# Kernel optimization log

Hardware: AMD Instinct MI355X
Metric: run time of the kernel (lower is better)

Reference implementation:

```python
import jax, jax.numpy as jnp
import numpy as np

EPS = 1e-5


def conv1x1(x, w, b=None):
    # x: [B,C,H,W], w: [O,C] (1x1 conv kernel squeezed)
    y = jnp.einsum('bchw,oc->bohw', x, w)
    if b is not None:
        y = y + b[None, :, None, None]
    return y


def bn_inf(x, g, b, m, v):
    scale = g / jnp.sqrt(v + EPS)
    return (x - m[None, :, None, None]) * scale[None, :, None, None] + b[None, :, None, None]


def setup_inputs() -> dict:
    B, C, H, W = 2, 256, 80, 80
    Ck, Cv, Co = 64, 128, 256
    key = jax.random.key(0)
    ks = jax.random.split(key, 16)
    d = {}
    d['x'] = jax.random.normal(ks[0], (B, C, H, W), dtype=jnp.float32)
    d['y'] = jax.random.normal(ks[1], (B, C, H, W), dtype=jnp.float32)
    s = 1.0 / np.sqrt(C)
    d['fk_w'] = jax.random.normal(ks[2], (Ck, C), dtype=jnp.float32) * s
    d['fk_g'] = jnp.ones((Ck,), jnp.float32)
    d['fk_b'] = jnp.zeros((Ck,), jnp.float32)
    d['fk_m'] = jax.random.normal(ks[3], (Ck,), dtype=jnp.float32) * 0.1
    d['fk_v'] = jax.random.uniform(ks[4], (Ck,), minval=0.5, maxval=1.5, dtype=jnp.float32)
    d['fq_w'] = jax.random.normal(ks[5], (Ck, C), dtype=jnp.float32) * s
    d['fq_g'] = jnp.ones((Ck,), jnp.float32)
    d['fq_b'] = jnp.zeros((Ck,), jnp.float32)
    d['fq_m'] = jax.random.normal(ks[6], (Ck,), dtype=jnp.float32) * 0.1
    d['fq_v'] = jax.random.uniform(ks[7], (Ck,), minval=0.5, maxval=1.5, dtype=jnp.float32)
    d['fv_w'] = jax.random.normal(ks[8], (Cv, C), dtype=jnp.float32) * s
    d['fv_b'] = jnp.zeros((Cv,), jnp.float32)
    d['W_w'] = jax.random.normal(ks[9], (Co, Cv), dtype=jnp.float32) * (1.0 / np.sqrt(Cv))
    d['W_b'] = jnp.zeros((Co,), jnp.float32)
    d['gamma'] = jnp.array([0.5], jnp.float32)
    return d


def reference(x, y, fk_w, fk_g, fk_b, fk_m, fk_v, fq_w, fq_g, fq_b, fq_m, fq_v, fv_w, fv_b, W_w, W_b, gamma):
    B, C, H, W = x.shape
    Ck = fk_w.shape[0]
    Cv = fv_w.shape[0]
    N = H * W
    # key from x, query/value from y (1x1 conv + BN projections)
    k = bn_inf(conv1x1(x, fk_w), fk_g, fk_b, fk_m, fk_v).reshape(B, Ck, N)          # [B,Ck,N]
    q = bn_inf(conv1x1(y, fq_w), fq_g, fq_b, fq_m, fq_v).reshape(B, Ck, N)          # [B,Ck,N]
    v = conv1x1(y, fv_w, fv_b).reshape(B, Cv, N)                                     # [B,Cv,N]
    sim = jnp.einsum('bkn,bkm->bnm', q, k) * (Ck ** -0.5)                            # [B,N,N]
    sim = jax.nn.softmax(sim, axis=-1)
    ctx = jnp.einsum('bnm,bvm->bvn', sim, v).reshape(B, Cv, H, W)                    # [B,Cv,H,W]
    ctx = conv1x1(ctx, W_w, W_b)                                                     # [B,Co,H,W]
    return gamma[0] * ctx + x
```

## Files before the change

kernel.cpp:

```cpp
#include <hip/hip_runtime.h>
#include <math.h>

#define NB   2
#define CIN  256
#define NN   6400
#define CKd  64
#define CVd  128
#define COd  256

using bf16   = __bf16;
using bf16x4 = __attribute__((ext_vector_type(4))) bf16;
using bf16x8 = __attribute__((ext_vector_type(8))) bf16;
using f32x4  = __attribute__((ext_vector_type(4))) float;

__device__ __forceinline__ void lds_cp16(const void* g, void* l) {
    __builtin_amdgcn_global_load_lds((const __attribute__((address_space(1))) void*)g,
                                     (__attribute__((address_space(3))) void*)l, 16, 0, 0);
}

__global__ void prep_kernel(const float* __restrict__ fk_w, const float* __restrict__ fk_g,
                            const float* __restrict__ fk_b, const float* __restrict__ fk_m,
                            const float* __restrict__ fk_v,
                            const float* __restrict__ fq_w, const float* __restrict__ fq_g,
                            const float* __restrict__ fq_b, const float* __restrict__ fq_m,
                            const float* __restrict__ fq_v,
                            const float* __restrict__ fv_w, const float* __restrict__ fv_b,
                            const float* __restrict__ W_w,  const float* __restrict__ W_b,
                            bf16* __restrict__ wkb, bf16* __restrict__ wqb,
                            bf16* __restrict__ wvb, bf16* __restrict__ wob,
                            float* __restrict__ bias)
{
    const int idx = blockIdx.x * 256 + threadIdx.x;
    const float QS = 0.18033688011112042f;
    if (idx < 16384) {
        const int co = idx >> 8;
        const float a = fk_g[co] * rsqrtf(fk_v[co] + 1e-5f);
        wkb[idx] = (bf16)(fk_w[idx] * a);
    } else if (idx < 32768) {
        const int i = idx - 16384, co = i >> 8;
        const float a = fq_g[co] * rsqrtf(fq_v[co] + 1e-5f) * QS;
        wqb[i] = (bf16)(fq_w[i] * a);
    } else if (idx < 65536) {
        const int i = idx - 32768;
        wvb[i] = (bf16)fv_w[i];
    } else if (idx < 98304) {
        const int i = idx - 65536;
        wob[i] = (bf16)W_w[i];
    } else if (idx < 98816) {
        const int j = idx - 98304;
        if (j < 64)       { const float a = fk_g[j] * rsqrtf(fk_v[j] + 1e-5f); bias[j] = fk_b[j] - fk_m[j] * a; }
        else if (j < 128) { const int c = j - 64; const float a = fq_g[c] * rsqrtf(fq_v[c] + 1e-5f); bias[j] = (fq_b[c] - fq_m[c] * a) * QS; }
        else if (j < 256) bias[j] = fv_b[j - 128];
        else              bias[j] = W_b[j - 256];
    }
}

__launch_bounds__(256, 4)
__global__ void projkqv_kernel(const float* __restrict__ x, const float* __restrict__ y,
                               const bf16* __restrict__ wkb, const bf16* __restrict__ wqb,
                               const bf16* __restrict__ wvb, const float* __restrict__ bias,
                               bf16* __restrict__ kb, bf16* __restrict__ qb, bf16* __restrict__ vb)
{
    __shared__ __align__(16) bf16 sbuf[64 * 128];
    __shared__ __align__(16) bf16 wbuf[64 * 128];

    const int tid  = threadIdx.x;
    const int lane = tid & 63, wav = tid >> 6;
    const int l15  = lane & 15, quad = lane >> 4;
    const int b    = blockIdx.z, m = blockIdx.y;
    const int n0   = blockIdx.x * 64;

    const float* srcg = ((m == 0) ? x : y) + (size_t)b * CIN * NN;
    const bf16* wg    = (m == 0) ? wkb : (m == 1) ? wqb : (wvb + (size_t)(m - 2) * 64 * CIN);

    const int key = l15 & 7;
    f32x4 acc[4];
#pragma unroll
    for (int j = 0; j < 4; ++j) acc[j] = (f32x4){0.f, 0.f, 0.f, 0.f};

    for (int p = 0; p < 2; ++p) {
        if (p) __syncthreads();

        {
            const int r4  = lane >> 4;
            const int c16 = lane & 15;
#pragma unroll
            for (int i = 0; i < 4; ++i) {
                const int rg = wav * 16 + i * 4;
                const int r  = rg + r4;
                const int cs = c16 ^ (r & 7);
                lds_cp16(wg + (size_t)r * 256 + p * 128 + cs * 8, &wbuf[rg * 128]);
            }
        }
        {
            const int nl = (tid & 15) * 4;
            const int cq = tid >> 4;
            const int cb = p * 128 + cq * 8;
            float4 v[8];
#pragma unroll
            for (int e = 0; e < 8; ++e)
                v[e] = *(const float4*)(srcg + (size_t)(cb + e) * NN + n0 + nl);
#pragma unroll
            for (int i = 0; i < 4; ++i) {
                const int n = nl + i;
                bf16x8 pk;
#pragma unroll
                for (int e = 0; e < 8; ++e) pk[e] = (bf16)(&v[e].x)[i];
                *(bf16x8*)&sbuf[n * 128 + ((cq ^ (n & 7)) * 8)] = pk;
            }
        }
        __syncthreads();

        if (m < 2) {
            const int arow = wav * 16 + l15;
#pragma unroll
            for (int k4 = 0; k4 < 16; k4 += 4) {
                const bf16x8 af = *(const bf16x8*)&sbuf[arow * 128 + (((k4 + quad) ^ key) * 8)];
#pragma unroll
                for (int nt = 0; nt < 4; ++nt) {
                    const int brow = nt * 16 + l15;
                    const bf16x8 bfw = *(const bf16x8*)&wbuf[brow * 128 + (((k4 + quad) ^ key) * 8)];
                    acc[nt] = __builtin_amdgcn_mfma_f32_16x16x32_bf16(af, bfw, acc[nt], 0, 0, 0);
                }
            }
        } else {
            const int arow = wav * 16 + l15;
#pragma unroll
            for (int k4 = 0; k4 < 16; k4 += 4) {
                const bf16x8 af = *(const bf16x8*)&wbuf[arow * 128 + (((k4 + quad) ^ key) * 8)];
#pragma unroll
                for (int nt = 0; nt < 4; ++nt) {
                    const int brow = nt * 16 + l15;
                    const bf16x8 bfy = *(const bf16x8*)&sbuf[brow * 128 + (((k4 + quad) ^ key) * 8)];
                    acc[nt] = __builtin_amdgcn_mfma_f32_16x16x32_bf16(af, bfy, acc[nt], 0, 0, 0);
                }
            }
        }
    }

    if (m < 2) {
        const float* bs = bias + m * 64;
        bf16* dst = (m == 0) ? kb : qb;
        const int nb = n0 + wav * 16;
#pragma unroll
        for (int nt = 0; nt < 4; ++nt) {
            const float bv = bs[nt * 16 + l15];
#pragma unroll
            for (int r = 0; r < 4; ++r) {
                const int n = nb + quad * 4 + r;
                dst[((size_t)b * NN + n) * CKd + nt * 16 + l15] = (bf16)(acc[nt][r] + bv);
            }
        }
    } else {
        const int cv0 = (m - 2) * 64 + wav * 16;
#pragma unroll
        for (int r = 0; r < 4; ++r) {
            const int cv = cv0 + quad * 4 + r;
            const float bv = bias[128 + cv];
#pragma unroll
            for (int nt = 0; nt < 4; ++nt)
                vb[((size_t)b * CVd + cv) * NN + n0 + nt * 16 + l15] = (bf16)(acc[nt][r] + bv);
        }
    }
}

__launch_bounds__(256, 2)
__global__ void attn_kernel(const bf16* __restrict__ qb, const bf16* __restrict__ kb,
                            const bf16* __restrict__ vb,
                            bf16* __restrict__ pO, float* __restrict__ pl, int KS)
{
    __shared__ __align__(16) bf16 kbuf[2][64 * 64];
    __shared__ __align__(16) bf16 vbuf[2][128 * 64];
    __shared__ __align__(16) bf16 p_lds[4][2][2][16][64];

    const int lane = threadIdx.x & 63;
    const int wav  = threadIdx.x >> 6;
    const int l15  = lane & 15;
    const int quad = lane >> 4;
    const int r8   = lane >> 3;
    const int c_src = (lane & 7) ^ r8;
    const int sw   = l15 & 7;
    const int pkey = (l15 & 7) << 1;

    const int id    = blockIdx.x;
    const int ks    = id % KS;
    const int rst   = id / KS;
    const int b     = rst & 1;
    const int qtile = rst >> 1;
    const int q0    = qtile * 256 + wav * 64;

    const bf16* qrow = qb + (size_t)b * NN * CKd;
    const bf16* krow = kb + (size_t)b * NN * CKd;
    const bf16* vrow = vb + (size_t)b * CVd * NN;

    bf16x8 qf[4][2];
#pragma unroll
    for (int qt = 0; qt < 4; ++qt)
#pragma unroll
        for (int s = 0; s < 2; ++s)
            qf[qt][s] = *(const bf16x8*)(qrow + (size_t)(q0 + qt * 16 + l15) * CKd + s * 32 + quad * 8);

    const float ZC = -11.541560327111707f;
    const f32x4 zini = (f32x4){ZC, ZC, ZC, ZC};

    f32x4 acc[4][8];
#pragma unroll
    for (int qt = 0; qt < 4; ++qt)
#pragma unroll
        for (int cv = 0; cv < 8; ++cv) acc[qt][cv] = (f32x4){0.f, 0.f, 0.f, 0.f};
    float psum[4] = {0.f, 0.f, 0.f, 0.f};

    const int t0 = (100 * ks) / KS;
    const int nt = (100 * (ks + 1)) / KS - t0;

    auto stage = [&](int t, int bi) {
        const int key0 = t * 64;
        lds_cp16(krow + (size_t)(key0 + wav * 8 + r8) * CKd + c_src * 8,
                 &kbuf[bi][(wav * 8) * 64]);
        lds_cp16(krow + (size_t)(key0 + (wav + 4) * 8 + r8) * CKd + c_src * 8,
                 &kbuf[bi][((wav + 4) * 8) * 64]);
#pragma unroll
        for (int g4 = 0; g4 < 4; ++g4) {
            const int g = wav * 4 + g4;
            lds_cp16(vrow + (size_t)(g * 8 + r8) * NN + key0 + c_src * 8,
                     &vbuf[bi][(g * 8) * 64]);
        }
    };

    stage(t0, 0);

    for (int t = 0; t < nt; ++t) {
        __syncthreads();
        if (t + 1 < nt) stage(t0 + t + 1, (t + 1) & 1);
        const bf16* kcur = &kbuf[t & 1][0];
        const bf16* vcur = &vbuf[t & 1][0];

        f32x4 s4[2][4];

        __builtin_amdgcn_s_setprio(1);
#pragma unroll
        for (int kt = 0; kt < 4; ++kt) {
            const int rr = kt * 16 + l15;
            const bf16x8 kf0 = *(const bf16x8*)&kcur[rr * 64 + ((quad ^ sw) * 8)];
            const bf16x8 kf1 = *(const bf16x8*)&kcur[rr * 64 + (((4 + quad) ^ sw) * 8)];
#pragma unroll
            for (int qtl = 0; qtl < 2; ++qtl) {
                f32x4 z = zini;
                z = __builtin_amdgcn_mfma_f32_16x16x32_bf16(kf0, qf[qtl][0], z, 0, 0, 0);
                z = __builtin_amdgcn_mfma_f32_16x16x32_bf16(kf1, qf[qtl][1], z, 0, 0, 0);
                s4[qtl][kt] = z;
            }
        }
        __builtin_amdgcn_s_setprio(0);

#pragma unroll
        for (int qtl = 0; qtl < 2; ++qtl) {
            float ps = 0.f;
#pragma unroll
            for (int kt = 0; kt < 4; ++kt) {
                bf16x4 pk;
#pragma unroll
                for (int r = 0; r < 4; ++r) {
                    const float p = exp2f(s4[qtl][kt][r]);
                    ps += p;
                    pk[r] = (bf16)p;
                }
                *(bf16x4*)&p_lds[wav][0][qtl][l15][((kt * 4 + quad) ^ pkey) * 4] = pk;
            }
            psum[qtl] += ps;
        }

        __builtin_amdgcn_s_setprio(1);
#pragma unroll
        for (int kt = 0; kt < 4; ++kt) {
            const int rr = kt * 16 + l15;
            const bf16x8 kf0 = *(const bf16x8*)&kcur[rr * 64 + ((quad ^ sw) * 8)];
            const bf16x8 kf1 = *(const bf16x8*)&kcur[rr * 64 + (((4 + quad) ^ sw) * 8)];
#pragma unroll
            for (int qtl = 0; qtl < 2; ++qtl) {
                f32x4 z = zini;
                z = __builtin_amdgcn_mfma_f32_16x16x32_bf16(kf0, qf[2 + qtl][0], z, 0, 0, 0);
                z = __builtin_amdgcn_mfma_f32_16x16x32_bf16(kf1, qf[2 + qtl][1], z, 0, 0, 0);
                s4[qtl][kt] = z;
            }
        }
        __builtin_amdgcn_s_setprio(0);

        {
            bf16x8 pfA, pfB;
#pragma unroll
            for (int u = 0; u < 8; ++u) {
                const int sp = u >> 2;
                if ((u & 3) == 0) {
                    pfA = *(const bf16x8*)&p_lds[wav][0][0][l15][((sp * 8 + quad * 2) ^ pkey) * 4];
                    pfB = *(const bf16x8*)&p_lds[wav][0][1][l15][((sp * 8 + quad * 2) ^ pkey) * 4];
                }
                {
                    const int qtl = u >> 2, kt = u & 3;
                    bf16x4 pk;
                    float ps = 0.f;
#pragma unroll
                    for (int r = 0; r < 4; ++r) {
                        const float p = exp2f(s4[qtl][kt][r]);
                        ps += p;
                        pk[r] = (bf16)p;
                    }
                    *(bf16x4*)&p_lds[wav][1][qtl][l15][((kt * 4 + quad) ^ pkey) * 4] = pk;
                    psum[2 + qtl] += ps;
                }
#pragma unroll
                for (int v2 = 0; v2 < 2; ++v2) {
                    const int cvt = (u & 3) * 2 + v2;
                    const int rr = cvt * 16 + l15;
                    const bf16x8 vf = *(const bf16x8*)&vcur[rr * 64 + (((sp * 4 + quad) ^ sw) * 8)];
                    acc[0][cvt] = __builtin_amdgcn_mfma_f32_16x16x32_bf16(vf, pfA, acc[0][cvt], 0, 0, 0);
                    acc[1][cvt] = __builtin_amdgcn_mfma_f32_16x16x32_bf16(vf, pfB, acc[1][cvt], 0, 0, 0);
                }
            }
        }

        __builtin_amdgcn_s_setprio(1);
#pragma unroll
        for (int sp = 0; sp < 2; ++sp) {
            const bf16x8 pf0 = *(const bf16x8*)&p_lds[wav][1][0][l15][((sp * 8 + quad * 2) ^ pkey) * 4];
            const bf16x8 pf1 = *(const bf16x8*)&p_lds[wav][1][1][l15][((sp * 8 + quad * 2) ^ pkey) * 4];
#pragma unroll
            for (int cvt = 0; cvt < 8; ++cvt) {
                const int rr = cvt * 16 + l15;
                const bf16x8 vf = *(const bf16x8*)&vcur[rr * 64 + (((sp * 4 + quad) ^ sw) * 8)];
                acc[2][cvt] = __builtin_amdgcn_mfma_f32_16x16x32_bf16(vf, pf0, acc[2][cvt], 0, 0, 0);
                acc[3][cvt] = __builtin_amdgcn_mfma_f32_16x16x32_bf16(vf, pf1, acc[3][cvt], 0, 0, 0);
            }
        }
        __builtin_amdgcn_s_setprio(0);
    }

    __syncthreads();
    bf16* tbuf = &p_lds[wav][0][0][0][0];
    const size_t pb = (size_t)ks * NB + b;
#pragma unroll
    for (int qt = 0; qt < 4; ++qt) {
        psum[qt] += __shfl_xor(psum[qt], 16);
        psum[qt] += __shfl_xor(psum[qt], 32);
#pragma unroll
        for (int cvt = 0; cvt < 8; ++cvt) {
            bf16x4 pk;
#pragma unroll
            for (int r = 0; r < 4; ++r) pk[r] = (bf16)acc[qt][cvt][r];
            const int u = (cvt * 4 + quad) ^ (l15 << 1);
            *(bf16x4*)&tbuf[l15 * 128 + u * 4] = pk;
        }
#pragma unroll
        for (int j = 0; j < 4; ++j) {
            const int row = j * 4 + (lane >> 4);
            const int g   = ((lane & 15) * 2) ^ ((row & 15) << 1);
            const bf16x8 vv = *(const bf16x8*)&tbuf[row * 128 + g * 4];
            *(bf16x8*)(pO + (pb * NN + q0 + qt * 16) * CVd + j * 512 + lane * 8) = vv;
        }
        if (quad == 0) pl[pb * NN + q0 + qt * 16 + l15] = psum[qt];
    }
}

__launch_bounds__(256, 4)
__global__ void outproj_kernel(const bf16* __restrict__ pO, const float* __restrict__ pl,
                               const bf16* __restrict__ wob, const float* __restrict__ bias,
                               const float* __restrict__ x, const float* __restrict__ gam,
                               float* __restrict__ out, int KS)
{
    __shared__ __align__(16) bf16 wbuf[128 * 128];
    __shared__ __align__(16) bf16 cbuf[32 * 128];

    const int tid  = threadIdx.x;
    const int lane = tid & 63, wav = tid >> 6;
    const int l15  = lane & 15, quad = lane >> 4;
    const int b    = blockIdx.y;
    const int n0   = blockIdx.x * 32;

    auto stage_w = [&](int p) {
        const int r4 = lane >> 4;
        const int c  = lane & 15;
#pragma unroll
        for (int i = 0; i < 8; ++i) {
            const int rg = wav * 32 + i * 4;
            const int r  = rg + r4;
            const int cs = c ^ (r & 7);
            lds_cp16(wob + (size_t)(p * 128 + r) * CVd + cs * 8, &wbuf[rg * 128]);
        }
    };
    stage_w(0);

    const int tn = tid >> 3;
    const int tc = (tid & 7) * 16;
    const size_t kstr = (size_t)NB * NN * CVd;
    const bf16* src0 = pO + ((size_t)b * NN + n0 + tn) * CVd + tc;
    float vacc[16];
#pragma unroll
    for (int i = 0; i < 16; ++i) vacc[i] = 0.f;
    float L = 0.f;

    bf16x8 c0 = *(const bf16x8*)(src0);
    bf16x8 c1 = *(const bf16x8*)(src0 + 8);
    for (int ksi = 0; ksi < KS; ++ksi) {
        bf16x8 nx0 = c0, nx1 = c1;
        if (ksi + 1 < KS) {
            const bf16* s = src0 + (size_t)(ksi + 1) * kstr;
            nx0 = *(const bf16x8*)(s);
            nx1 = *(const bf16x8*)(s + 8);
        }
        L += pl[(size_t)(ksi * NB + b) * NN + n0 + tn];
#pragma unroll
        for (int e = 0; e < 8; ++e) vacc[e]     += (float)c0[e];
#pragma unroll
        for (int e = 0; e < 8; ++e) vacc[8 + e] += (float)c1[e];
        c0 = nx0; c1 = nx1;
    }
    {
        const float rL = 1.0f / L;
#pragma unroll
        for (int j = 0; j < 2; ++j) {
            bf16x8 o;
#pragma unroll
            for (int e = 0; e < 8; ++e) o[e] = (bf16)(vacc[j * 8 + e] * rL);
            const int c = (tid & 7) * 2 + j;
            *(bf16x8*)&cbuf[tn * 128 + ((c ^ (tn & 7)) * 8)] = o;
        }
    }
    __syncthreads();

    const float gm = gam[0];

    auto mfma_pass = [&](f32x4 (&acc)[2][2]) {
#pragma unroll
        for (int i = 0; i < 2; ++i)
#pragma unroll
            for (int j = 0; j < 2; ++j) acc[i][j] = (f32x4){0.f, 0.f, 0.f, 0.f};
#pragma unroll
        for (int kk = 0; kk < 4; ++kk) {
#pragma unroll
            for (int cot = 0; cot < 2; ++cot) {
                const int arow = wav * 32 + cot * 16 + l15;
                const bf16x8 af = *(const bf16x8*)&wbuf[arow * 128 + (((kk * 4 + quad) ^ (arow & 7)) * 8)];
#pragma unroll
                for (int nt = 0; nt < 2; ++nt) {
                    const int brow = nt * 16 + l15;
                    const bf16x8 bfc = *(const bf16x8*)&cbuf[brow * 128 + (((kk * 4 + quad) ^ (brow & 7)) * 8)];
                    acc[cot][nt] = __builtin_amdgcn_mfma_f32_16x16x32_bf16(af, bfc, acc[cot][nt], 0, 0, 0);
                }
            }
        }
    };
    auto store_pass = [&](const f32x4 (&acc)[2][2], int p) {
#pragma unroll
        for (int cot = 0; cot < 2; ++cot)
#pragma unroll
            for (int r = 0; r < 4; ++r) {
                const int co = p * 128 + wav * 32 + cot * 16 + quad * 4 + r;
                const float bv = bias[256 + co];
#pragma unroll
                for (int nt = 0; nt < 2; ++nt) {
                    const int n = n0 + nt * 16 + l15;
                    const size_t a = ((size_t)b * COd + co) * NN + n;
                    out[a] = gm * (acc[cot][nt][r] + bv) + x[a];
                }
            }
    };

    f32x4 acc0[2][2];
    mfma_pass(acc0);
    __syncthreads();
    stage_w(1);
    store_pass(acc0, 0);
    __syncthreads();
    f32x4 acc1[2][2];
    mfma_pass(acc1);
    store_pass(acc1, 1);
}

extern "C" void kernel_launch(void* const* d_in, const int* in_sizes, int n_in,
                              void* d_out, int out_size, void* d_ws, size_t ws_size,
                              hipStream_t stream)
{
    const float* x     = (const float*)d_in[0];
    const float* y     = (const float*)d_in[1];
    const float* fk_w  = (const float*)d_in[2];
    const float* fk_g  = (const float*)d_in[3];
    const float* fk_b  = (const float*)d_in[4];
    const float* fk_m  = (const float*)d_in[5];
    const float* fk_v  = (const float*)d_in[6];
    const float* fq_w  = (const float*)d_in[7];
    const float* fq_g  = (const float*)d_in[8];
    const float* fq_b  = (const float*)d_in[9];
    const float* fq_m  = (const float*)d_in[10];
    const float* fq_v  = (const float*)d_in[11];
    const float* fv_w  = (const float*)d_in[12];
    const float* fv_b  = (const float*)d_in[13];
    const float* W_w   = (const float*)d_in[14];
    const float* W_b   = (const float*)d_in[15];
    const float* gamma = (const float*)d_in[16];
    float* out = (float*)d_out;

    char* ws = (char*)d_ws;
    size_t off = 0;
    auto carve = [&](size_t bytes) -> char* {
        char* p = ws + off;
        off = (off + bytes + 255) & ~(size_t)255;
        return p;
    };

    bf16*  kb   = (bf16*)carve((size_t)NB * NN * CKd * 2);
    bf16*  qbuf = (bf16*)carve((size_t)NB * NN * CKd * 2);
    bf16*  vb   = (bf16*)carve((size_t)NB * CVd * NN * 2);
    bf16*  wkb  = (bf16*)carve((size_t)CKd * CIN * 2);
    bf16*  wqb  = (bf16*)carve((size_t)CKd * CIN * 2);
    bf16*  wvb  = (bf16*)carve((size_t)CVd * CIN * 2);
    bf16*  wob  = (bf16*)carve((size_t)COd * CVd * 2);
    float* bias = (float*)carve(512 * 4);

    const size_t region = ws_size - off;
    const size_t per_ks = (size_t)NB * NN * CVd * 2 + (size_t)NB * NN * 4 + 512;
    int KS = 1;
    {
        const int cand[6] = {10, 8, 5, 4, 2, 1};
        for (int i = 0; i < 6; ++i)
            if ((size_t)cand[i] * per_ks <= region) { KS = cand[i]; break; }
    }
    bf16*  pO = (bf16*)carve((size_t)KS * NB * NN * CVd * 2);
    float* pl = (float*)carve((size_t)KS * NB * NN * 4);

    const dim3 blk(256);
    prep_kernel<<<386, blk, 0, stream>>>(fk_w, fk_g, fk_b, fk_m, fk_v,
                                         fq_w, fq_g, fq_b, fq_m, fq_v,
                                         fv_w, fv_b, W_w, W_b,
                                         wkb, wqb, wvb, wob, bias);
    projkqv_kernel<<<dim3(100, 4, NB), blk, 0, stream>>>(x, y, wkb, wqb, wvb, bias, kb, qbuf, vb);
    attn_kernel<<<dim3(25 * NB * KS), blk, 0, stream>>>(qbuf, kb, vb, pO, pl, KS);
    outproj_kernel<<<dim3(200, NB), blk, 0, stream>>>(pO, pl, wob, bias, x, gamma, out, KS);
}
```

Baseline: 172.6 us.

## Fuse weight prep into projection kernels and simplify attention inner loop schedule

Removes the separate prep kernel and instead has the projection and output-projection kernels read fp32 weights directly, fold in the BN scale and bias, and convert to bf16 while staging into LDS. This saves one kernel launch and the round trip through global memory for the converted weights, but every block now redoes the conversion and uses plain register loads instead of async direct-to-LDS copies. Separately, the attention loop drops its hand-interleaved softmax/PV pipelining and setprio hints in favor of a simpler two-phase loop with a halved P buffer, with the max offset applied as a subtraction. The simpler loop may lose the overlap of exp and MFMA work that the old schedule provided.

```diff
diff --git a/kernel.cpp b/kernel.cpp
--- a/kernel.cpp
+++ b/kernel.cpp
@@ -18,47 +18,15 @@
                                      (__attribute__((address_space(3))) void*)l, 16, 0, 0);
 }
 
-__global__ void prep_kernel(const float* __restrict__ fk_w, const float* __restrict__ fk_g,
-                            const float* __restrict__ fk_b, const float* __restrict__ fk_m,
-                            const float* __restrict__ fk_v,
-                            const float* __restrict__ fq_w, const float* __restrict__ fq_g,
-                            const float* __restrict__ fq_b, const float* __restrict__ fq_m,
-                            const float* __restrict__ fq_v,
-                            const float* __restrict__ fv_w, const float* __restrict__ fv_b,
-                            const float* __restrict__ W_w,  const float* __restrict__ W_b,
-                            bf16* __restrict__ wkb, bf16* __restrict__ wqb,
-                            bf16* __restrict__ wvb, bf16* __restrict__ wob,
-                            float* __restrict__ bias)
-{
-    const int idx = blockIdx.x * 256 + threadIdx.x;
-    const float QS = 0.18033688011112042f;
-    if (idx < 16384) {
-        const int co = idx >> 8;
-        const float a = fk_g[co] * rsqrtf(fk_v[co] + 1e-5f);
-        wkb[idx] = (bf16)(fk_w[idx] * a);
-    } else if (idx < 32768) {
-        const int i = idx - 16384, co = i >> 8;
-        const float a = fq_g[co] * rsqrtf(fq_v[co] + 1e-5f) * QS;
-        wqb[i] = (bf16)(fq_w[i] * a);
-    } else if (idx < 65536) {
-        const int i = idx - 32768;
-        wvb[i] = (bf16)fv_w[i];
-    } else if (idx < 98304) {
-        const int i = idx - 65536;
-        wob[i] = (bf16)W_w[i];
-    } else if (idx < 98816) {
-        const int j = idx - 98304;
-        if (j < 64)       { const float a = fk_g[j] * rsqrtf(fk_v[j] + 1e-5f); bias[j] = fk_b[j] - fk_m[j] * a; }
-        else if (j < 128) { const int c = j - 64; const float a = fq_g[c] * rsqrtf(fq_v[c] + 1e-5f); bias[j] = (fq_b[c] - fq_m[c] * a) * QS; }
-        else if (j < 256) bias[j] = fv_b[j - 128];
-        else              bias[j] = W_b[j - 256];
-    }
-}
-
 __launch_bounds__(256, 4)
 __global__ void projkqv_kernel(const float* __restrict__ x, const float* __restrict__ y,
-                               const bf16* __restrict__ wkb, const bf16* __restrict__ wqb,
-                               const bf16* __restrict__ wvb, const float* __restrict__ bias,
+                               const float* __restrict__ fk_w, const float* __restrict__ fk_g,
+                               const float* __restrict__ fk_b, const float* __restrict__ fk_m,
+                               const float* __restrict__ fk_v,
+                               const float* __restrict__ fq_w, const float* __restrict__ fq_g,
+                               const float* __restrict__ fq_b, const float* __restrict__ fq_m,
+                               const float* __restrict__ fq_v,
+                               const float* __restrict__ fv_w, const float* __restrict__ fv_b,
                                bf16* __restrict__ kb, bf16* __restrict__ qb, bf16* __restrict__ vb)
 {
     __shared__ __align__(16) bf16 sbuf[64 * 128];
@@ -69,9 +37,9 @@
     const int l15  = lane & 15, quad = lane >> 4;
     const int b    = blockIdx.z, m = blockIdx.y;
     const int n0   = blockIdx.x * 64;
+    const float QS = 0.18033688011112042f;
 
     const float* srcg = ((m == 0) ? x : y) + (size_t)b * CIN * NN;
-    const bf16* wg    = (m == 0) ? wkb : (m == 1) ? wqb : (wvb + (size_t)(m - 2) * 64 * CIN);
 
     const int key = l15 & 7;
     f32x4 acc[4];
@@ -86,10 +54,22 @@
             const int c16 = lane & 15;
 #pragma unroll
             for (int i = 0; i < 4; ++i) {
-                const int rg = wav * 16 + i * 4;
-                const int r  = rg + r4;
+                const int r  = wav * 16 + i * 4 + r4;
                 const int cs = c16 ^ (r & 7);
-                lds_cp16(wg + (size_t)r * 256 + p * 128 + cs * 8, &wbuf[rg * 128]);
+                const float* ws = (m == 0) ? (fk_w + (size_t)r * CIN)
+                                : (m == 1) ? (fq_w + (size_t)r * CIN)
+                                : (fv_w + (size_t)((m - 2) * 64 + r) * CIN);
+                const float4 w0 = *(const float4*)(ws + p * 128 + cs * 8);
+                const float4 w1 = *(const float4*)(ws + p * 128 + cs * 8 + 4);
+                float a = 1.0f;
+                if (m == 0)      a = fk_g[r] * rsqrtf(fk_v[r] + 1e-5f);
+                else if (m == 1) a = fq_g[r] * rsqrtf(fq_v[r] + 1e-5f) * QS;
+                bf16x8 pk;
+                pk[0] = (bf16)(w0.x * a); pk[1] = (bf16)(w0.y * a);
+                pk[2] = (bf16)(w0.z * a); pk[3] = (bf16)(w0.w * a);
+                pk[4] = (bf16)(w1.x * a); pk[5] = (bf16)(w1.y * a);
+                pk[6] = (bf16)(w1.z * a); pk[7] = (bf16)(w1.w * a);
+                *(bf16x8*)&wbuf[r * 128 + c16 * 8] = pk;
             }
         }
         {
@@ -139,12 +119,21 @@
     }
 
     if (m < 2) {
-        const float* bs = bias + m * 64;
         bf16* dst = (m == 0) ? kb : qb;
         const int nb = n0 + wav * 16;
 #pragma unroll
         for (int nt = 0; nt < 4; ++nt) {
-            const float bv = bs[nt * 16 + l15];
+            float bv;
+            {
+                const int c = nt * 16 + l15;
+                if (m == 0) {
+                    const float a = fk_g[c] * rsqrtf(fk_v[c] + 1e-5f);
+                    bv = fk_b[c] - fk_m[c] * a;
+                } else {
+                    const float a = fq_g[c] * rsqrtf(fq_v[c] + 1e-5f);
+                    bv = (fq_b[c] - fq_m[c] * a) * QS;
+                }
+            }
 #pragma unroll
             for (int r = 0; r < 4; ++r) {
                 const int n = nb + quad * 4 + r;
@@ -156,7 +145,7 @@
 #pragma unroll
         for (int r = 0; r < 4; ++r) {
             const int cv = cv0 + quad * 4 + r;
-            const float bv = bias[128 + cv];
+            const float bv = fv_b[cv];
 #pragma unroll
             for (int nt = 0; nt < 4; ++nt)
                 vb[((size_t)b * CVd + cv) * NN + n0 + nt * 16 + l15] = (bf16)(acc[nt][r] + bv);
@@ -171,7 +160,7 @@
 {
     __shared__ __align__(16) bf16 kbuf[2][64 * 64];
     __shared__ __align__(16) bf16 vbuf[2][128 * 64];
-    __shared__ __align__(16) bf16 p_lds[4][2][2][16][64];
+    __shared__ __align__(16) bf16 p_lds[4][2][16][64];
 
     const int lane = threadIdx.x & 63;
     const int wav  = threadIdx.x >> 6;
@@ -200,9 +189,6 @@
         for (int s = 0; s < 2; ++s)
             qf[qt][s] = *(const bf16x8*)(qrow + (size_t)(q0 + qt * 16 + l15) * CKd + s * 32 + quad * 8);
 
-    const float ZC = -11.541560327111707f;
-    const f32x4 zini = (f32x4){ZC, ZC, ZC, ZC};
-
     f32x4 acc[4][8];
 #pragma unroll
     for (int qt = 0; qt < 4; ++qt)
@@ -235,108 +221,58 @@
         const bf16* kcur = &kbuf[t & 1][0];
         const bf16* vcur = &vbuf[t & 1][0];
 
-        f32x4 s4[2][4];
-
-        __builtin_amdgcn_s_setprio(1);
-#pragma unroll
-        for (int kt = 0; kt < 4; ++kt) {
-            const int rr = kt * 16 + l15;
-            const bf16x8 kf0 = *(const bf16x8*)&kcur[rr * 64 + ((quad ^ sw) * 8)];
-            const bf16x8 kf1 = *(const bf16x8*)&kcur[rr * 64 + (((4 + quad) ^ sw) * 8)];
+#pragma unroll
+        for (int ph = 0; ph < 2; ++ph) {
+            f32x4 s4[2][4];
+#pragma unroll
+            for (int kt = 0; kt < 4; ++kt) {
+                const int rr = kt * 16 + l15;
+                const bf16x8 kf0 = *(const bf16x8*)&kcur[rr * 64 + ((quad ^ sw) * 8)];
+                const bf16x8 kf1 = *(const bf16x8*)&kcur[rr * 64 + (((4 + quad) ^ sw) * 8)];
+#pragma unroll
+                for (int qtl = 0; qtl < 2; ++qtl) {
+                    const int qt = ph * 2 + qtl;
+                    f32x4 z = (f32x4){0.f, 0.f, 0.f, 0.f};
+                    z = __builtin_amdgcn_mfma_f32_16x16x32_bf16(kf0, qf[qt][0], z, 0, 0, 0);
+                    z = __builtin_amdgcn_mfma_f32_16x16x32_bf16(kf1, qf[qt][1], z, 0, 0, 0);
+                    s4[qtl][kt] = z;
+                }
+            }
+
 #pragma unroll
             for (int qtl = 0; qtl < 2; ++qtl) {
-                f32x4 z = zini;
-                z = __builtin_amdgcn_mfma_f32_16x16x32_bf16(kf0, qf[qtl][0], z, 0, 0, 0);
-                z = __builtin_amdgcn_mfma_f32_16x16x32_bf16(kf1, qf[qtl][1], z, 0, 0, 0);
-                s4[qtl][kt] = z;
-            }
-        }
-        __builtin_amdgcn_s_setprio(0);
-
-#pragma unroll
-        for (int qtl = 0; qtl < 2; ++qtl) {
-            float ps = 0.f;
-#pragma unroll
-            for (int kt = 0; kt < 4; ++kt) {
-                bf16x4 pk;
-#pragma unroll
-                for (int r = 0; r < 4; ++r) {
-                    const float p = exp2f(s4[qtl][kt][r]);
-                    ps += p;
-                    pk[r] = (bf16)p;
-                }
-                *(bf16x4*)&p_lds[wav][0][qtl][l15][((kt * 4 + quad) ^ pkey) * 4] = pk;
-            }
-            psum[qtl] += ps;
-        }
-
-        __builtin_amdgcn_s_setprio(1);
-#pragma unroll
-        for (int kt = 0; kt < 4; ++kt) {
-            const int rr = kt * 16 + l15;
-            const bf16x8 kf0 = *(const bf16x8*)&kcur[rr * 64 + ((quad ^ sw) * 8)];
-            const bf16x8 kf1 = *(const bf16x8*)&kcur[rr * 64 + (((4 + quad) ^ sw) * 8)];
-#pragma unroll
-            for (int qtl = 0; qtl < 2; ++qtl) {
-                f32x4 z = zini;
-                z = __builtin_amdgcn_mfma_f32_16x16x32_bf16(kf0, qf[2 + qtl][0], z, 0, 0, 0);
-                z = __builtin_amdgcn_mfma_f32_16x16x32_bf16(kf1, qf[2 + qtl][1], z, 0, 0, 0);
-                s4[qtl][kt] = z;
-            }
-        }
-        __builtin_amdgcn_s_setprio(0);
-
-        {
-            bf16x8 pfA, pfB;
-#pragma unroll
-            for (int u = 0; u < 8; ++u) {
-                const int sp = u >> 2;
-                if ((u & 3) == 0) {
-                    pfA = *(const bf16x8*)&p_lds[wav][0][0][l15][((sp * 8 + quad * 2) ^ pkey) * 4];
-                    pfB = *(const bf16x8*)&p_lds[wav][0][1][l15][((sp * 8 + quad * 2) ^ pkey) * 4];
-                }
-                {
-                    const int qtl = u >> 2, kt = u & 3;
+                float ps = 0.f;
+#pragma unroll
+                for (int kt = 0; kt < 4; ++kt) {
                     bf16x4 pk;
-                    float ps = 0.f;
 #pragma unroll
                     for (int r = 0; r < 4; ++r) {
-                        const float p = exp2f(s4[qtl][kt][r]);
+                        const float p = exp2f(s4[qtl][kt][r] - 11.541560327111707f);
                         ps += p;
                         pk[r] = (bf16)p;
                     }
-                    *(bf16x4*)&p_lds[wav][1][qtl][l15][((kt * 4 + quad) ^ pkey) * 4] = pk;
-                    psum[2 + qtl] += ps;
-                }
-#pragma unroll
-                for (int v2 = 0; v2 < 2; ++v2) {
-                    const int cvt = (u & 3) * 2 + v2;
+                    *(bf16x4*)&p_lds[wav][qtl][l15][((kt * 4 + quad) ^ pkey) * 4] = pk;
+                }
+                psum[ph * 2 + qtl] += ps;
+            }
+
+#pragma unroll
+            for (int sp = 0; sp < 2; ++sp) {
+                const bf16x8 pf0 = *(const bf16x8*)&p_lds[wav][0][l15][((sp * 8 + quad * 2) ^ pkey) * 4];
+                const bf16x8 pf1 = *(const bf16x8*)&p_lds[wav][1][l15][((sp * 8 + quad * 2) ^ pkey) * 4];
+#pragma unroll
+                for (int cvt = 0; cvt < 8; ++cvt) {
                     const int rr = cvt * 16 + l15;
                     const bf16x8 vf = *(const bf16x8*)&vcur[rr * 64 + (((sp * 4 + quad) ^ sw) * 8)];
-                    acc[0][cvt] = __builtin_amdgcn_mfma_f32_16x16x32_bf16(vf, pfA, acc[0][cvt], 0, 0, 0);
-                    acc[1][cvt] = __builtin_amdgcn_mfma_f32_16x16x32_bf16(vf, pfB, acc[1][cvt], 0, 0, 0);
-                }
-            }
-        }
-
-        __builtin_amdgcn_s_setprio(1);
-#pragma unroll
-        for (int sp = 0; sp < 2; ++sp) {
-            const bf16x8 pf0 = *(const bf16x8*)&p_lds[wav][1][0][l15][((sp * 8 + quad * 2) ^ pkey) * 4];
-            const bf16x8 pf1 = *(const bf16x8*)&p_lds[wav][1][1][l15][((sp * 8 + quad * 2) ^ pkey) * 4];
-#pragma unroll
-            for (int cvt = 0; cvt < 8; ++cvt) {
-                const int rr = cvt * 16 + l15;
-                const bf16x8 vf = *(const bf16x8*)&vcur[rr * 64 + (((sp * 4 + quad) ^ sw) * 8)];
-                acc[2][cvt] = __builtin_amdgcn_mfma_f32_16x16x32_bf16(vf, pf0, acc[2][cvt], 0, 0, 0);
-                acc[3][cvt] = __builtin_amdgcn_mfma_f32_16x16x32_bf16(vf, pf1, acc[3][cvt], 0, 0, 0);
-            }
-        }
-        __builtin_amdgcn_s_setprio(0);
+                    acc[ph * 2 + 0][cvt] = __builtin_amdgcn_mfma_f32_16x16x32_bf16(vf, pf0, acc[ph * 2 + 0][cvt], 0, 0, 0);
+                    acc[ph * 2 + 1][cvt] = __builtin_amdgcn_mfma_f32_16x16x32_bf16(vf, pf1, acc[ph * 2 + 1][cvt], 0, 0, 0);
+                }
+            }
+        }
     }
 
     __syncthreads();
-    bf16* tbuf = &p_lds[wav][0][0][0][0];
+    bf16* tbuf = &p_lds[wav][0][0][0];
     const size_t pb = (size_t)ks * NB + b;
 #pragma unroll
     for (int qt = 0; qt < 4; ++qt) {
@@ -363,7 +299,7 @@
 
 __launch_bounds__(256, 4)
 __global__ void outproj_kernel(const bf16* __restrict__ pO, const float* __restrict__ pl,
-                               const bf16* __restrict__ wob, const float* __restrict__ bias,
+                               const float* __restrict__ W_w, const float* __restrict__ W_b,
                                const float* __restrict__ x, const float* __restrict__ gam,
                                float* __restrict__ out, int KS)
 {
@@ -378,13 +314,18 @@
 
     auto stage_w = [&](int p) {
         const int r4 = lane >> 4;
-        const int c  = lane & 15;
+        const int c16 = lane & 15;
 #pragma unroll
         for (int i = 0; i < 8; ++i) {
-            const int rg = wav * 32 + i * 4;
-            const int r  = rg + r4;
-            const int cs = c ^ (r & 7);
-            lds_cp16(wob + (size_t)(p * 128 + r) * CVd + cs * 8, &wbuf[rg * 128]);
+            const int r  = wav * 32 + i * 4 + r4;
+            const int cs = c16 ^ (r & 7);
+            const float* ws = W_w + (size_t)(p * 128 + r) * CVd + cs * 8;
+            const float4 w0 = *(const float4*)(ws);
+            const float4 w1 = *(const float4*)(ws + 4);
+            bf16x8 pk;
+            pk[0] = (bf16)w0.x; pk[1] = (bf16)w0.y; pk[2] = (bf16)w0.z; pk[3] = (bf16)w0.w;
+            pk[4] = (bf16)w1.x; pk[5] = (bf16)w1.y; pk[6] = (bf16)w1.z; pk[7] = (bf16)w1.w;
+            *(bf16x8*)&wbuf[r * 128 + c16 * 8] = pk;
         }
     };
     stage_w(0);
@@ -455,7 +396,7 @@
 #pragma unroll
             for (int r = 0; r < 4; ++r) {
                 const int co = p * 128 + wav * 32 + cot * 16 + quad * 4 + r;
-                const float bv = bias[256 + co];
+                const float bv = W_b[co];
 #pragma unroll
                 for (int nt = 0; nt < 2; ++nt) {
                     const int n = n0 + nt * 16 + l15;
@@ -510,11 +451,6 @@
     bf16*  kb   = (bf16*)carve((size_t)NB * NN * CKd * 2);
     bf16*  qbuf = (bf16*)carve((size_t)NB * NN * CKd * 2);
     bf16*  vb   = (bf16*)carve((size_t)NB * CVd * NN * 2);
-    bf16*  wkb  = (bf16*)carve((size_t)CKd * CIN * 2);
-    bf16*  wqb  = (bf16*)carve((size_t)CKd * CIN * 2);
-    bf16*  wvb  = (bf16*)carve((size_t)CVd * CIN * 2);
-    bf16*  wob  = (bf16*)carve((size_t)COd * CVd * 2);
-    float* bias = (float*)carve(512 * 4);
 
     const size_t region = ws_size - off;
     const size_t per_ks = (size_t)NB * NN * CVd * 2 + (size_t)NB * NN * 4 + 512;
@@ -528,11 +464,10 @@
     float* pl = (float*)carve((size_t)KS * NB * NN * 4);
 
     const dim3 blk(256);
-    prep_kernel<<<386, blk, 0, stream>>>(fk_w, fk_g, fk_b, fk_m, fk_v,
-                                         fq_w, fq_g, fq_b, fq_m, fq_v,
-                                         fv_w, fv_b, W_w, W_b,
-                                         wkb, wqb, wvb, wob, bias);
-    projkqv_kernel<<<dim3(100, 4, NB), blk, 0, stream>>>(x, y, wkb, wqb, wvb, bias, kb, qbuf, vb);
+    projkqv_kernel<<<dim3(100, 4, NB), blk, 0, stream>>>(x, y,
+                                                         fk_w, fk_g, fk_b, fk_m, fk_v,
+                                                         fq_w, fq_g, fq_b, fq_m, fq_v,
+                                                         fv_w, fv_b, kb, qbuf, vb);
     attn_kernel<<<dim3(25 * NB * KS), blk, 0, stream>>>(qbuf, kb, vb, pO, pl, KS);
-    outproj_kernel<<<dim3(200, NB), blk, 0, stream>>>(pO, pl, wob, bias, x, gamma, out, KS);
+    outproj_kernel<<<dim3(200, NB), blk, 0, stream>>>(pO, pl, W_w, W_b, x, gamma, out, KS);
 }
```

After: 170.9 us. Within noise of the previous version (-0.9%).
